# Kernel tuning notes

Measured on AMD Instinct MI355X. Metric: run time of the kernel, lower is better.

The kernel has to match this reference:

```python
import jax, jax.numpy as jnp
import numpy as np
import math

B, S, D, H = 2, 2048, 1024, 16
HD = D // H
KL_GAMMA = 0.1
EPS = 1e-10


def setup_inputs() -> dict:
    key = jax.random.key(0)
    ks = jax.random.split(key, 12)
    # positive inputs + positive weights keep scores > 0 so log(mean(scores)) is finite
    query = jax.random.uniform(ks[0], (B, S, D), dtype=jnp.float32)
    k_in = jax.random.uniform(ks[1], (B, S, D), dtype=jnp.float32)
    v_in = jax.random.uniform(ks[2], (B, S, D), dtype=jnp.float32)
    def w(k):
        return jax.random.uniform(k, (D, D), dtype=jnp.float32) * 0.002
    b = jnp.full((D,), 1e-3, dtype=jnp.float32)
    return {
        "query": query, "key": k_in, "value": v_in,
        "Wq": w(ks[3]), "bq": b,
        "Wk": w(ks[4]), "bk": b,
        "Wv": w(ks[5]), "bv": b,
        "Wo": w(ks[6]), "bo": b,
    }


def reference(query, key, value, Wq, bq, Wk, bk, Wv, bv, Wo, bo):
    Bq, Sq, _ = query.shape
    Sk = key.shape[1]
    # projections, split heads: [B, H, S, HD]
    Q = (query @ Wq + bq).reshape(Bq, Sq, H, HD).transpose(0, 2, 1, 3)
    K = (key @ Wk + bk).reshape(Bq, Sk, H, HD).transpose(0, 2, 1, 3)
    V = (value @ Wv + bv).reshape(Bq, Sk, H, HD).transpose(0, 2, 1, 3)
    scores = jnp.einsum("bhqd,bhkd->bhqk", Q, K) / math.sqrt(HD)  # [B,H,Sq,Sk]
    # KL bias: row-mean broadcast over keys, then log
    target = jnp.mean(scores, axis=-1, keepdims=True)  # [B,H,Sq,1]
    scores = scores + KL_GAMMA * jnp.log(target + EPS)
    attn = jax.nn.softmax(scores, axis=-1)
    ctx = jnp.einsum("bhqk,bhkd->bhqd", attn, V)
    ctx = ctx.transpose(0, 2, 1, 3).reshape(Bq, Sq, D)
    return ctx @ Wo + bo
```

## Files before the change

### kernel.cpp

```cpp
#include <hip/hip_runtime.h>
#include <hip/hip_bf16.h>
#include <stdint.h>


#define NB 2
#define NS 2048
#define ND 1024
#define NH 16
#define HD 64

typedef short bf16x8 __attribute__((ext_vector_type(8)));
typedef short bf16x4 __attribute__((ext_vector_type(4)));
typedef float f32x4 __attribute__((ext_vector_type(4)));
typedef float f32x16 __attribute__((ext_vector_type(16)));
typedef unsigned int u32x4 __attribute__((ext_vector_type(4)));

static __device__ __forceinline__ short f2bf(float f) {
    uint32_t u = __builtin_bit_cast(uint32_t, f);
    uint32_t r = (u + 0x7fffu + ((u >> 16) & 1u)) >> 16;
    return (short)(uint16_t)r;
}

static __device__ __forceinline__ unsigned int cvtpk(float lo, float hi) {
    unsigned int r;
    asm("v_cvt_pk_bf16_f32 %0, %1, %2" : "=v"(r) : "v"(lo), "v"(hi));
    return r;
}

#if __has_builtin(__builtin_amdgcn_exp2f)
#define EXP2(x) __builtin_amdgcn_exp2f(x)
#else
#define EXP2(x) exp2f(x)
#endif

static __device__ __forceinline__ void plswap(unsigned& a, unsigned& b) {
#if __has_builtin(__builtin_amdgcn_permlane32_swap)
    auto r = __builtin_amdgcn_permlane32_swap(a, b, false, false);
    a = r[0]; b = r[1];
#else
    const int l = (int)(threadIdx.x & 63);
    unsigned bl = __shfl(b, l & 31);
    unsigned ah = __shfl(a, (l & 31) + 32);
    a = (l < 32) ? a : bl;
    b = (l < 32) ? ah : b;
#endif
}

typedef __attribute__((address_space(1))) const unsigned int glob_u32;
typedef __attribute__((address_space(3))) unsigned int lds_u32;
static __device__ __forceinline__ void gload16(const void* g, void* l) {
    __builtin_amdgcn_global_load_lds((glob_u32*)g, (lds_u32*)l, 16, 0, 0);
}

__global__ __launch_bounds__(256) void prep_cast(const float* __restrict__ q,
                                                 const float* __restrict__ k,
                                                 const float* __restrict__ v,
                                                 short* __restrict__ Qo,
                                                 short* __restrict__ Ko,
                                                 short* __restrict__ Vo) {
    const float* src = (blockIdx.z == 0) ? q : (blockIdx.z == 1) ? k : v;
    short* dst = (blockIdx.z == 0) ? Qo : (blockIdx.z == 1) ? Ko : Vo;
    const size_t i = ((size_t)blockIdx.x * 256 + threadIdx.x) * 8;
    f32x4 a = *(const f32x4*)(src + i);
    f32x4 b = *(const f32x4*)(src + i + 4);
    bf16x8 o;
    o[0] = f2bf(a[0]); o[1] = f2bf(a[1]); o[2] = f2bf(a[2]); o[3] = f2bf(a[3]);
    o[4] = f2bf(b[0]); o[5] = f2bf(b[1]); o[6] = f2bf(b[2]); o[7] = f2bf(b[3]);
    *(bf16x8*)(dst + i) = o;
}

__global__ __launch_bounds__(256) void prep_wt(const float* __restrict__ W0,
                                               const float* __restrict__ W1,
                                               const float* __restrict__ W2,
                                               const float* __restrict__ W3,
                                               short* __restrict__ WtAll) {
    __shared__ short tile[32][33];
    const float* W = (blockIdx.z == 0) ? W0 : (blockIdx.z == 1) ? W1
                   : (blockIdx.z == 2) ? W2 : W3;
    short* Wt = WtAll + (size_t)blockIdx.z * (ND * ND);
    const int tx = threadIdx.x & 31;
    const int ty = threadIdx.x >> 5;
    const int k0 = blockIdx.x * 32, n0 = blockIdx.y * 32;
#pragma unroll
    for (int i = 0; i < 4; i++)
        tile[ty + i * 8][tx] = f2bf(W[(size_t)(k0 + ty + i * 8) * ND + n0 + tx]);
    __syncthreads();
#pragma unroll
    for (int i = 0; i < 4; i++)
        Wt[(size_t)(n0 + ty + i * 8) * ND + k0 + tx] = tile[tx][ty + i * 8];
}

static __device__ __forceinline__ void gemm_body(const short* __restrict__ A,
                                                 const short* __restrict__ Wt,
                                                 const float* __restrict__ bias,
                                                 void* __restrict__ Out,
                                                 int mode, float scale,
                                                 char* As2, char* Bs2) {
    const int tid = threadIdx.x;
    const int gm = blockIdx.x * 128;
    const int gn = blockIdx.y * 128;
    const int w = tid >> 6;
    const int l = tid & 63;
    const int r = l & 15;
    const int g = l >> 4;
    const int wr = w >> 1, wc = w & 1;

    f32x4 acc[4][4];
#pragma unroll
    for (int m = 0; m < 4; m++)
#pragma unroll
        for (int n = 0; n < 4; n++) acc[m][n] = (f32x4){0.f, 0.f, 0.f, 0.f};

    const int lin = ((w * 2) << 10) + l * 16;
#pragma unroll
    for (int j = 0; j < 2; j++) {
        const int lj = lin + (j << 10);
        const int row = lj >> 6;
        const int colL = (lj & 63) ^ (((row ^ (row >> 2)) & 3) << 4);
        gload16((const char*)A + (size_t)(gm + row) * (ND * 2) + colL, As2 + lj);
        gload16((const char*)Wt + (size_t)(gn + row) * (ND * 2) + colL, Bs2 + lj);
    }
    __syncthreads();

    for (int t = 0; t < ND / 32; t++) {
        const int cur = (t & 1) << 13;
        const int nxt = cur ^ 8192;
        if (t < ND / 32 - 1) {
            const int k0b = (t + 1) * 64;
#pragma unroll
            for (int j = 0; j < 2; j++) {
                const int lj = lin + (j << 10);
                const int row = lj >> 6;
                const int colL = (lj & 63) ^ (((row ^ (row >> 2)) & 3) << 4);
                gload16((const char*)A + (size_t)(gm + row) * (ND * 2) + k0b + colL,
                        As2 + nxt + lj);
                gload16((const char*)Wt + (size_t)(gn + row) * (ND * 2) + k0b + colL,
                        Bs2 + nxt + lj);
            }
        }
        bf16x8 af[4], bfv[4];
#pragma unroll
        for (int m = 0; m < 4; m++) {
            const int ar = wr * 64 + m * 16 + r;
            const int fa = ((ar ^ (ar >> 2)) & 3) << 4;
            af[m] = *(const bf16x8*)(As2 + cur + ar * 64 + ((g << 4) ^ fa));
        }
#pragma unroll
        for (int n = 0; n < 4; n++) {
            const int br = wc * 64 + n * 16 + r;
            const int fb = ((br ^ (br >> 2)) & 3) << 4;
            bfv[n] = *(const bf16x8*)(Bs2 + cur + br * 64 + ((g << 4) ^ fb));
        }
#pragma unroll
        for (int m = 0; m < 4; m++)
#pragma unroll
            for (int n = 0; n < 4; n++)
                acc[m][n] = __builtin_amdgcn_mfma_f32_16x16x32_bf16(
                    af[m], bfv[n], acc[m][n], 0, 0, 0);
        __syncthreads();
    }

#pragma unroll
    for (int m = 0; m < 4; m++) {
        const int orow = gm + wr * 64 + m * 16 + g * 4;
#pragma unroll
        for (int n = 0; n < 4; n++) {
            const int ocol = gn + wc * 64 + n * 16 + r;
            const float bv = bias[ocol];
#pragma unroll
            for (int i = 0; i < 4; i++) {
                const float vout = (acc[m][n][i] + bv) * scale;
                const int row = orow + i;
                if (mode == 0) {
                    const int b = row >> 11, s = row & 2047;
                    const int h = ocol >> 6, hd = ocol & 63;
                    ((short*)Out)[(((size_t)(b * NH + h) * NS + s) << 6) + hd] = f2bf(vout);
                } else if (mode == 1) {
                    const int b = row >> 11, s = row & 2047;
                    const int h = ocol >> 6, hd = ocol & 63;
                    ((short*)Out)[((size_t)(b * NH + h) * HD + hd) * NS + s] = f2bf(vout);
                } else {
                    ((float*)Out)[(size_t)row * ND + ocol] = vout;
                }
            }
        }
    }
}

#define QSCALE 0.18033688011112042f

__global__ __launch_bounds__(256, 3) void gemm_qkv(const short* __restrict__ Qin,
                                                   const short* __restrict__ Kin,
                                                   const short* __restrict__ Vin,
                                                   const short* __restrict__ WtAll,
                                                   const float* __restrict__ bq,
                                                   const float* __restrict__ bk,
                                                   const float* __restrict__ bv,
                                                   short* __restrict__ Qo,
                                                   short* __restrict__ Ko,
                                                   short* __restrict__ Vto) {
    __shared__ __align__(16) char As[2 * 8192];
    __shared__ __align__(16) char Bs[2 * 8192];
    const int z = blockIdx.z;
    const short* A = (z == 0) ? Qin : (z == 1) ? Kin : Vin;
    const short* Wt = WtAll + (size_t)z * ND * ND;
    const float* bias = (z == 0) ? bq : (z == 1) ? bk : bv;
    void* Out = (z == 0) ? (void*)Qo : (z == 1) ? (void*)Ko : (void*)Vto;
    const float scale = (z == 0) ? QSCALE : 1.0f;
    const int mode = (z == 2) ? 1 : 0;
    gemm_body(A, Wt, bias, Out, mode, scale, As, Bs);
}

__global__ __launch_bounds__(256, 3) void gemm_fin(const short* __restrict__ Ctx,
                                                   const short* __restrict__ Wt,
                                                   const float* __restrict__ bo,
                                                   float* __restrict__ Out) {
    __shared__ __align__(16) char As[2 * 8192];
    __shared__ __align__(16) char Bs[2 * 8192];
    gemm_body(Ctx, Wt, bo, Out, 2, 1.0f, As, Bs);
}

static __device__ __forceinline__ void stage2(const char* Kp8, const char* Vp8,
                                              char* Kbuf, char* Vbuf,
                                              int t, int w, int l) {
#pragma unroll
    for (int jj = 0; jj < 2; jj++) {
        const int chunk = w * 2 + jj;
        const int half = chunk >> 3;
        const int lin = ((chunk & 7) << 10) + l * 16;
        const int sw = lin ^ (((lin >> 7) & 7) << 4);
        const int row = sw >> 7, col = sw & 127;
        gload16(Kp8 + (size_t)(half * 1024 + t * 64 + row) * 128 + col,
                Kbuf + half * 8192 + ((chunk & 7) << 10));
        gload16(Vp8 + (size_t)row * (NS * 2) + (half * 1024 + t * 64) * 2 + col,
                Vbuf + half * 8192 + ((chunk & 7) << 10));
    }
}

__global__ __launch_bounds__(512, 2) void attn_kern(const short* __restrict__ Q,
                                                    const short* __restrict__ K,
                                                    const short* __restrict__ Vt,
                                                    short* __restrict__ Ctx) {
    __shared__ __align__(16) char smem[2][2][16384];
    __shared__ float rsbuf[8][2][32];

    const int tid = threadIdx.x;
    const int w = tid >> 6;
    const int l = tid & 63;
    const int c = l & 31;
    const int h = l >> 5;
    const int h16 = h << 4;

    const int bid = blockIdx.x;
    const int swb = (bid & 7) * 32 + (bid >> 3);
    const int bh = swb >> 3;
    const int qt = swb & 7;
    const int g = w & 3;
    const int khalf = w >> 2;
    const int qw = qt * 256 + g * 64;

    const short* Qp = Q + (size_t)bh * NS * HD;
    const char* Kp8 = (const char*)(K + (size_t)bh * NS * HD);
    const char* Vp8 = (const char*)(Vt + (size_t)bh * HD * NS);

    bf16x8 qf[2][4];
#pragma unroll
    for (int qc = 0; qc < 2; qc++)
#pragma unroll
        for (int st = 0; st < 4; st++)
            qf[qc][st] = *(const bf16x8*)(Qp + (size_t)(qw + qc * 32 + c) * HD +
                                          st * 16 + h * 8);

    f32x16 acc[2][2];
#pragma unroll
    for (int qc = 0; qc < 2; qc++)
#pragma unroll
        for (int dt = 0; dt < 2; dt++) acc[qc][dt] = (f32x16)(0.f);
    float rs0 = 0.f, rs1 = 0.f;

    const int sx = (c & 7) << 4;

    stage2(Kp8, Vp8, smem[0][0], smem[0][1], 0, w, l);
    __syncthreads();

    int bufi = 0;
    for (int t = 0; t < 16; t++) {
        if (t < 15)
            stage2(Kp8, Vp8, smem[bufi ^ 1][0], smem[bufi ^ 1][1], t + 1, w, l);

        const char* Kt = smem[bufi][0] + khalf * 8192;
        const char* Vv = smem[bufi][1] + khalf * 8192;

#pragma unroll
        for (int ktile = 0; ktile < 2; ktile++) {
            bf16x8 kf[4];
#pragma unroll
            for (int st = 0; st < 4; st++)
                kf[st] = *(const bf16x8*)(Kt + ((ktile * 32 + c) << 7) +
                                          ((st * 32 + h16) ^ sx));
            f32x16 S0 = (f32x16)(0.f), S1 = (f32x16)(0.f);
#pragma unroll
            for (int st = 0; st < 4; st++) {
                S0 = __builtin_amdgcn_mfma_f32_32x32x16_bf16(kf[st], qf[0][st], S0, 0, 0, 0);
                S1 = __builtin_amdgcn_mfma_f32_32x32x16_bf16(kf[st], qf[1][st], S1, 0, 0, 0);
            }

            float tv0[16], tv1[16];
#pragma unroll
            for (int i = 0; i < 16; i++) {
                tv0[i] = EXP2(S0[i]); rs0 += tv0[i];
                tv1[i] = EXP2(S1[i]); rs1 += tv1[i];
            }
            unsigned p0a[4], p0b[4], p1a[4], p1b[4];
#pragma unroll
            for (int q4 = 0; q4 < 4; q4++) {
                p0a[q4] = cvtpk(tv0[4 * q4], tv0[4 * q4 + 1]);
                p0b[q4] = cvtpk(tv0[4 * q4 + 2], tv0[4 * q4 + 3]);
                p1a[q4] = cvtpk(tv1[4 * q4], tv1[4 * q4 + 1]);
                p1b[q4] = cvtpk(tv1[4 * q4 + 2], tv1[4 * q4 + 3]);
            }

#pragma unroll
            for (int ks = 0; ks < 2; ks++) {
                unsigned a0 = p0a[2 * ks], b0 = p0a[2 * ks + 1];
                unsigned a1 = p0b[2 * ks], b1 = p0b[2 * ks + 1];
                plswap(a0, b0); plswap(a1, b1);
                u32x4 pw0; pw0[0] = a0; pw0[1] = a1; pw0[2] = b0; pw0[3] = b1;
                bf16x8 pa0 = __builtin_bit_cast(bf16x8, pw0);
                unsigned c0 = p1a[2 * ks], d0 = p1a[2 * ks + 1];
                unsigned c1 = p1b[2 * ks], d1 = p1b[2 * ks + 1];
                plswap(c0, d0); plswap(c1, d1);
                u32x4 pw1; pw1[0] = c0; pw1[1] = c1; pw1[2] = d0; pw1[3] = d1;
                bf16x8 pa1 = __builtin_bit_cast(bf16x8, pw1);
#pragma unroll
                for (int dt = 0; dt < 2; dt++) {
                    bf16x8 vb = *(const bf16x8*)(Vv + ((dt * 32 + c) << 7) +
                                                 ((ktile * 64 + ks * 32 + h16) ^ sx));
                    acc[0][dt] = __builtin_amdgcn_mfma_f32_32x32x16_bf16(pa0, vb, acc[0][dt], 0, 0, 0);
                    acc[1][dt] = __builtin_amdgcn_mfma_f32_32x32x16_bf16(pa1, vb, acc[1][dt], 0, 0, 0);
                }
            }
        }
        __syncthreads();
        bufi ^= 1;
    }

    rs0 += __shfl_xor(rs0, 32);
    rs1 += __shfl_xor(rs1, 32);
    if (h == 0) { rsbuf[w][0][c] = rs0; rsbuf[w][1][c] = rs1; }

    float* sumbuf = (float*)&smem[0][0][0];
    if (w >= 4) {
#pragma unroll
        for (int qc = 0; qc < 2; qc++)
#pragma unroll
            for (int q4 = 0; q4 < 4; q4++)
#pragma unroll
                for (int i = 0; i < 4; i++) {
                    const int qrow = qc * 32 + i + 8 * q4 + 4 * h;
#pragma unroll
                    for (int dt = 0; dt < 2; dt++)
                        sumbuf[((g * 64 + qrow) << 6) + dt * 32 + c] =
                            acc[qc][dt][q4 * 4 + i];
                }
    }
    __syncthreads();
    if (w < 4) {
        const int b = bh >> 4, hh = bh & 15;
#pragma unroll
        for (int qc = 0; qc < 2; qc++)
#pragma unroll
            for (int q4 = 0; q4 < 4; q4++)
#pragma unroll
                for (int i = 0; i < 4; i++) {
                    const int qrow32 = i + 8 * q4 + 4 * h;
                    const int qrow = qc * 32 + qrow32;
                    const float inv = 1.0f / (rsbuf[g][qc][qrow32] +
                                              rsbuf[4 + g][qc][qrow32]);
                    short* op = Ctx + ((size_t)b * NS + qt * 256 + g * 64 + qrow) * ND +
                                hh * HD;
#pragma unroll
                    for (int dt = 0; dt < 2; dt++) {
                        const float val = acc[qc][dt][q4 * 4 + i] +
                                          sumbuf[((g * 64 + qrow) << 6) + dt * 32 + c];
                        op[dt * 32 + c] = f2bf(val * inv);
                    }
                }
    }
}

extern "C" void kernel_launch(void* const* d_in, const int* in_sizes, int n_in,
                              void* d_out, int out_size, void* d_ws, size_t ws_size,
                              hipStream_t stream) {
    (void)in_sizes; (void)n_in; (void)out_size; (void)ws_size;
    const float* query = (const float*)d_in[0];
    const float* key_  = (const float*)d_in[1];
    const float* value = (const float*)d_in[2];
    const float* Wq = (const float*)d_in[3];
    const float* bq = (const float*)d_in[4];
    const float* Wk = (const float*)d_in[5];
    const float* bk = (const float*)d_in[6];
    const float* Wv = (const float*)d_in[7];
    const float* bv = (const float*)d_in[8];
    const float* Wo = (const float*)d_in[9];
    const float* bo = (const float*)d_in[10];

    char* ws = (char*)d_ws;
    const size_t MB = 1024 * 1024;
    short* WtAll = (short*)ws;
    short* Qin = (short*)(ws + 8 * MB);
    short* Kin = (short*)(ws + 16 * MB);
    short* Vin = (short*)(ws + 24 * MB);
    short* Qb  = (short*)(ws + 32 * MB);
    short* Kb  = (short*)(ws + 40 * MB);
    short* Vtb = (short*)(ws + 48 * MB);
    short* Ctx = (short*)(ws + 8 * MB);

    prep_cast<<<dim3(2048, 1, 3), 256, 0, stream>>>(query, key_, value, Qin, Kin, Vin);
    prep_wt<<<dim3(32, 32, 4), 256, 0, stream>>>(Wq, Wk, Wv, Wo, WtAll);
    gemm_qkv<<<dim3(32, 8, 3), 256, 0, stream>>>(Qin, Kin, Vin, WtAll, bq, bk, bv,
                                                 Qb, Kb, Vtb);
    attn_kern<<<dim3(256), 512, 0, stream>>>(Qb, Kb, Vtb, Ctx);
    gemm_fin<<<dim3(32, 8), 256, 0, stream>>>(Ctx, WtAll + 3 * ND * ND, bo, (float*)d_out);
}
```

Baseline: 119.1 us.

## Triple-buffer GEMM LDS loads and use counted vmcnt waits in attention loop

The projection GEMMs move from double to triple buffering of LDS tiles, issuing loads two k-steps ahead and waiting with explicit s_waitcnt vmcnt counts instead of a full drain before each barrier. The attention kernel's K/V staging loop likewise waits only for the previous stage's loads, so the prefetch of the next tile stays in flight during compute. The aim is to hide global-to-LDS latency better. In exchange, the GEMMs use more shared memory, which may reduce occupancy under launch_bounds(256,3), and the hand-counted vmcnt values must match the number of loads issued or results will be wrong.

```diff
diff --git a/kernel.cpp b/kernel.cpp
--- a/kernel.cpp
+++ b/kernel.cpp
@@ -51,6 +51,11 @@
 static __device__ __forceinline__ void gload16(const void* g, void* l) {
     __builtin_amdgcn_global_load_lds((glob_u32*)g, (lds_u32*)l, 16, 0, 0);
 }
+
+#define VMW(N) do { asm volatile("s_waitcnt vmcnt(" #N ")" ::: "memory"); \
+                    __builtin_amdgcn_sched_barrier(0); } while (0)
+#define BAR()  do { __builtin_amdgcn_s_barrier();                          \
+                    __builtin_amdgcn_sched_barrier(0); } while (0)
 
 __global__ __launch_bounds__(256) void prep_cast(const float* __restrict__ q,
                                                  const float* __restrict__ k,
@@ -90,12 +95,52 @@
         Wt[(size_t)(n0 + ty + i * 8) * ND + k0 + tx] = tile[tx][ty + i * 8];
 }
 
+static __device__ __forceinline__ void gemm_stage(const char* A, const char* W,
+                                                  char* As3, char* Bs3,
+                                                  int buf, int tile,
+                                                  int gm, int gn, int lin) {
+#pragma unroll
+    for (int j = 0; j < 2; j++) {
+        const int lj = lin + (j << 10);
+        const int row = lj >> 6;
+        const int colL = (lj & 63) ^ (((row ^ (row >> 2)) & 3) << 4);
+        gload16(A + (size_t)(gm + row) * (ND * 2) + tile * 64 + colL,
+                As3 + buf * 8192 + lj);
+        gload16(W + (size_t)(gn + row) * (ND * 2) + tile * 64 + colL,
+                Bs3 + buf * 8192 + lj);
+    }
+}
+
+static __device__ __forceinline__ void gemm_step(const char* AsB, const char* BsB,
+                                                 int wr, int wc, int r, int g,
+                                                 f32x4 (&acc)[4][4]) {
+    bf16x8 af[4], bfv[4];
+#pragma unroll
+    for (int m = 0; m < 4; m++) {
+        const int ar = wr * 64 + m * 16 + r;
+        const int fa = ((ar ^ (ar >> 2)) & 3) << 4;
+        af[m] = *(const bf16x8*)(AsB + ar * 64 + ((g << 4) ^ fa));
+    }
+#pragma unroll
+    for (int n = 0; n < 4; n++) {
+        const int br = wc * 64 + n * 16 + r;
+        const int fb = ((br ^ (br >> 2)) & 3) << 4;
+        bfv[n] = *(const bf16x8*)(BsB + br * 64 + ((g << 4) ^ fb));
+    }
+#pragma unroll
+    for (int m = 0; m < 4; m++)
+#pragma unroll
+        for (int n = 0; n < 4; n++)
+            acc[m][n] = __builtin_amdgcn_mfma_f32_16x16x32_bf16(
+                af[m], bfv[n], acc[m][n], 0, 0, 0);
+}
+
 static __device__ __forceinline__ void gemm_body(const short* __restrict__ A,
                                                  const short* __restrict__ Wt,
                                                  const float* __restrict__ bias,
                                                  void* __restrict__ Out,
                                                  int mode, float scale,
-                                                 char* As2, char* Bs2) {
+                                                 char* As3, char* Bs3) {
     const int tid = threadIdx.x;
     const int gm = blockIdx.x * 128;
     const int gn = blockIdx.y * 128;
@@ -104,6 +149,8 @@
     const int r = l & 15;
     const int g = l >> 4;
     const int wr = w >> 1, wc = w & 1;
+    const char* Ap = (const char*)A;
+    const char* Wp = (const char*)Wt;
 
     f32x4 acc[4][4];
 #pragma unroll
@@ -112,53 +159,28 @@
         for (int n = 0; n < 4; n++) acc[m][n] = (f32x4){0.f, 0.f, 0.f, 0.f};
 
     const int lin = ((w * 2) << 10) + l * 16;
-#pragma unroll
-    for (int j = 0; j < 2; j++) {
-        const int lj = lin + (j << 10);
-        const int row = lj >> 6;
-        const int colL = (lj & 63) ^ (((row ^ (row >> 2)) & 3) << 4);
-        gload16((const char*)A + (size_t)(gm + row) * (ND * 2) + colL, As2 + lj);
-        gload16((const char*)Wt + (size_t)(gn + row) * (ND * 2) + colL, Bs2 + lj);
-    }
-    __syncthreads();
-
-    for (int t = 0; t < ND / 32; t++) {
-        const int cur = (t & 1) << 13;
-        const int nxt = cur ^ 8192;
-        if (t < ND / 32 - 1) {
-            const int k0b = (t + 1) * 64;
-#pragma unroll
-            for (int j = 0; j < 2; j++) {
-                const int lj = lin + (j << 10);
-                const int row = lj >> 6;
-                const int colL = (lj & 63) ^ (((row ^ (row >> 2)) & 3) << 4);
-                gload16((const char*)A + (size_t)(gm + row) * (ND * 2) + k0b + colL,
-                        As2 + nxt + lj);
-                gload16((const char*)Wt + (size_t)(gn + row) * (ND * 2) + k0b + colL,
-                        Bs2 + nxt + lj);
-            }
-        }
-        bf16x8 af[4], bfv[4];
-#pragma unroll
-        for (int m = 0; m < 4; m++) {
-            const int ar = wr * 64 + m * 16 + r;
-            const int fa = ((ar ^ (ar >> 2)) & 3) << 4;
-            af[m] = *(const bf16x8*)(As2 + cur + ar * 64 + ((g << 4) ^ fa));
-        }
-#pragma unroll
-        for (int n = 0; n < 4; n++) {
-            const int br = wc * 64 + n * 16 + r;
-            const int fb = ((br ^ (br >> 2)) & 3) << 4;
-            bfv[n] = *(const bf16x8*)(Bs2 + cur + br * 64 + ((g << 4) ^ fb));
-        }
-#pragma unroll
-        for (int m = 0; m < 4; m++)
-#pragma unroll
-            for (int n = 0; n < 4; n++)
-                acc[m][n] = __builtin_amdgcn_mfma_f32_16x16x32_bf16(
-                    af[m], bfv[n], acc[m][n], 0, 0, 0);
-        __syncthreads();
-    }
+
+    gemm_stage(Ap, Wp, As3, Bs3, 0, 0, gm, gn, lin);
+    gemm_stage(Ap, Wp, As3, Bs3, 1, 1, gm, gn, lin);
+
+    int cur = 0, stg = 2;
+    for (int t = 0; t < ND / 32 - 2; t++) {
+        gemm_stage(Ap, Wp, As3, Bs3, stg, t + 2, gm, gn, lin);
+        VMW(8);
+        BAR();
+        gemm_step(As3 + cur * 8192, Bs3 + cur * 8192, wr, wc, r, g, acc);
+        BAR();
+        cur = (cur == 2) ? 0 : cur + 1;
+        stg = (stg == 2) ? 0 : stg + 1;
+    }
+    VMW(4);
+    BAR();
+    gemm_step(As3 + cur * 8192, Bs3 + cur * 8192, wr, wc, r, g, acc);
+    BAR();
+    cur = (cur == 2) ? 0 : cur + 1;
+    VMW(0);
+    BAR();
+    gemm_step(As3 + cur * 8192, Bs3 + cur * 8192, wr, wc, r, g, acc);
 
 #pragma unroll
     for (int m = 0; m < 4; m++) {
@@ -199,8 +221,8 @@
                                                    short* __restrict__ Qo,
                                                    short* __restrict__ Ko,
                                                    short* __restrict__ Vto) {
-    __shared__ __align__(16) char As[2 * 8192];
-    __shared__ __align__(16) char Bs[2 * 8192];
+    __shared__ __align__(16) char As[3 * 8192];
+    __shared__ __align__(16) char Bs[3 * 8192];
     const int z = blockIdx.z;
     const short* A = (z == 0) ? Qin : (z == 1) ? Kin : Vin;
     const short* Wt = WtAll + (size_t)z * ND * ND;
@@ -215,8 +237,8 @@
                                                    const short* __restrict__ Wt,
                                                    const float* __restrict__ bo,
                                                    float* __restrict__ Out) {
-    __shared__ __align__(16) char As[2 * 8192];
-    __shared__ __align__(16) char Bs[2 * 8192];
+    __shared__ __align__(16) char As[3 * 8192];
+    __shared__ __align__(16) char Bs[3 * 8192];
     gemm_body(Ctx, Wt, bo, Out, 2, 1.0f, As, Bs);
 }
 
@@ -281,12 +303,17 @@
     const int sx = (c & 7) << 4;
 
     stage2(Kp8, Vp8, smem[0][0], smem[0][1], 0, w, l);
-    __syncthreads();
 
     int bufi = 0;
+#pragma unroll 1
     for (int t = 0; t < 16; t++) {
-        if (t < 15)
+        if (t < 15) {
             stage2(Kp8, Vp8, smem[bufi ^ 1][0], smem[bufi ^ 1][1], t + 1, w, l);
+            VMW(4);
+        } else {
+            VMW(0);
+        }
+        BAR();
 
         const char* Kt = smem[bufi][0] + khalf * 8192;
         const char* Vv = smem[bufi][1] + khalf * 8192;
@@ -341,7 +368,7 @@
                 }
             }
         }
-        __syncthreads();
+        BAR();
         bufi ^= 1;
     }
 
```

Measured after the change: 118.2 us. About the same (-0.8%).
